# Performance work log

Hardware: AMD Instinct MI355X
Metric: run time of the kernel (lower is better)

The kernel has to match this reference:

```python
import jax, jax.numpy as jnp
import numpy as np

H = 256  # hidden_size


def _lstm_cell(x, h, c, Wih, Whh, b):
    # PyTorch gate order: input, forget, cell(g), output
    gates = x @ Wih.T + h @ Whh.T + b  # (B, 4H)
    i, f, g, o = jnp.split(gates, 4, axis=-1)
    c_new = jax.nn.sigmoid(f) * c + jax.nn.sigmoid(i) * jnp.tanh(g)
    h_new = jax.nn.sigmoid(o) * jnp.tanh(c_new)
    return h_new, c_new


def setup_inputs() -> dict:
    key = jax.random.key(0)
    ks = jax.random.split(key, 9)
    B, D_in, T, H4 = 64, 64, 1024, 4 * H
    s = 0.05  # keep gates out of saturation
    return {
        "x": jax.random.normal(ks[0], (B, D_in, T), jnp.float32),
        # layer 0: input size 64; layers 1-2: input size 2*H (bidirectional concat)
        "Wih0": jax.random.normal(ks[1], (2, H4, D_in), jnp.float32) * s,
        "Whh0": jax.random.normal(ks[2], (2, H4, H), jnp.float32) * s,
        "b0": jax.random.normal(ks[3], (2, H4), jnp.float32) * s,  # b_ih + b_hh fused
        "Wih12": jax.random.normal(ks[4], (2, 2, H4, 2 * H), jnp.float32) * s,
        "Whh12": jax.random.normal(ks[5], (2, 2, H4, H), jnp.float32) * s,
        "b12": jax.random.normal(ks[6], (2, 2, H4), jnp.float32) * s,
        # Conv1d(1, 81, (256,1)) == per-timestep linear over the hidden dim
        "conv_w": jax.random.normal(ks[7], (81, H), jnp.float32) * s,
        "conv_b": jax.random.normal(ks[8], (81,), jnp.float32) * s,
    }


def reference(x, Wih0, Whh0, b0, Wih12, Whh12, b12, conv_w, conv_b):
    B = x.shape[0]
    seq = jnp.transpose(x, (2, 0, 1))  # (T, B, D_in) like x.permute(2,0,1)
    h0 = jnp.zeros((6, B, H), x.dtype)  # num_layers * num_directions = 6
    c0 = jnp.zeros((6, B, H), x.dtype)

    def step(carry, x_t):
        h, c = carry
        hs, cs = [], []
        inp = x_t  # single timestep fed to the (bi)LSTM: both dirs see the same input
        for l in range(3):
            outs = []
            for d in range(2):
                idx = 2 * l + d
                if l == 0:
                    Wih, Whh, b = Wih0[d], Whh0[d], b0[d]
                else:
                    Wih, Whh, b = Wih12[l - 1, d], Whh12[l - 1, d], b12[l - 1, d]
                hn, cn = _lstm_cell(inp, h[idx], c[idx], Wih, Whh, b)
                outs.append(hn)
                hs.append(hn)
                cs.append(cn)
            inp = jnp.concatenate(outs, axis=-1)  # (B, 2H) into next layer
        new_h = jnp.stack(hs)
        new_c = jnp.stack(cs)
        # h.view(L, 2, B, H)[-1, -1]: last layer, backward direction
        return (new_h, new_c), hs[-1]

    _, ys = jax.lax.scan(step, (h0, c0), seq)  # ys: (T, B, H)

    # y.permute(1,2,0).unsqueeze(1) -> conv (256,1) kernel -> squeeze(2):
    # logits[b, o, t] = sum_h conv_w[o, h] * ys[t, b, h] + conv_b[o]
    logits = jnp.einsum('tbh,oh->bot', ys, conv_w) + conv_b[None, :, None]
    probs = jax.nn.softmax(logits, axis=1)
    return jnp.argmax(probs, axis=1)  # (B, T) int
```

## Files before the change

### kernel.cpp

```cpp
#include <hip/hip_runtime.h>


#define H_ 256
#define B_ 64
#define T_ 1024
#define NBLK 256
#define NTHR 1024
#define HBUF 98304
#define NTICK 1026

#define OFF_GEN  0
#define OFF_ROOT 64
#define OFF_CNT  128
#define OFF_H    4096
#define OFF_XT   1048576
#define OFF_YS   17825792

__device__ __forceinline__ float sigf(float x) {
  return 1.0f / (1.0f + __expf(-x));
}
__device__ __forceinline__ float tanhf_(float x) {
  float e = __expf(-2.0f * fabsf(x));
  float r = (1.0f - e) / (1.0f + e);
  return x >= 0.0f ? r : -r;
}

__device__ __forceinline__ void llc_ld1(const float4* p, float4& r) {
  asm volatile(
      "global_load_dwordx4 %0, %1, off sc0 sc1\n\t"
      "s_waitcnt vmcnt(0)"
      : "=v"(r)
      : "v"(p)
      : "memory");
}
__device__ __forceinline__ void llc_ld4(const float4* p, float4& r0, float4& r1,
                                        float4& r2, float4& r3) {
  asm volatile(
      "global_load_dwordx4 %0, %4, off sc0 sc1\n\t"
      "global_load_dwordx4 %1, %4, off offset:1024 sc0 sc1\n\t"
      "global_load_dwordx4 %2, %4, off offset:2048 sc0 sc1\n\t"
      "global_load_dwordx4 %3, %4, off offset:3072 sc0 sc1\n\t"
      "s_waitcnt vmcnt(0)"
      : "=&v"(r0), "=&v"(r1), "=&v"(r2), "=&v"(r3)
      : "v"(p)
      : "memory");
}
__device__ __forceinline__ void llc_ld8(const float4* p, const float4* q,
                                        float4& r0, float4& r1, float4& r2,
                                        float4& r3, float4& r4, float4& r5,
                                        float4& r6, float4& r7) {
  asm volatile(
      "global_load_dwordx4 %0, %8, off sc0 sc1\n\t"
      "global_load_dwordx4 %1, %8, off offset:1024 sc0 sc1\n\t"
      "global_load_dwordx4 %2, %8, off offset:2048 sc0 sc1\n\t"
      "global_load_dwordx4 %3, %8, off offset:3072 sc0 sc1\n\t"
      "global_load_dwordx4 %4, %9, off sc0 sc1\n\t"
      "global_load_dwordx4 %5, %9, off offset:1024 sc0 sc1\n\t"
      "global_load_dwordx4 %6, %9, off offset:2048 sc0 sc1\n\t"
      "global_load_dwordx4 %7, %9, off offset:3072 sc0 sc1\n\t"
      "s_waitcnt vmcnt(0)"
      : "=&v"(r0), "=&v"(r1), "=&v"(r2), "=&v"(r3), "=&v"(r4), "=&v"(r5),
        "=&v"(r6), "=&v"(r7)
      : "v"(p), "v"(q)
      : "memory");
}
__device__ __forceinline__ void llc_st_f2(float* p, float2 v) {
  asm volatile("global_store_dwordx2 %0, %1, off sc0 sc1" ::"v"(p), "v"(v)
               : "memory");
}

__global__ __launch_bounds__(64) void transpose_x(const float* __restrict__ x,
                                                  float* __restrict__ xT) {
  __shared__ float tile[64][65];
  const int k = blockIdx.y;
  const int t0 = blockIdx.x * 64;
  const int lane = threadIdx.x;
  for (int bi = 0; bi < 64; ++bi)
    tile[bi][lane] = x[bi * 65536 + k * 1024 + t0 + lane];
  __syncthreads();
  for (int ti = 0; ti < 64; ++ti)
    xT[(size_t)(t0 + ti) * 4096 + (k >> 2) * 256 + lane * 4 + (k & 3)] =
        tile[lane][ti];
}

__device__ __forceinline__ void body8(float* __restrict__ acc, const float4 av,
                                      const float* __restrict__ wl,
                                      const int k4) {
  const float* wp = wl + (size_t)k4 * 32;
#pragma unroll
  for (int a = 0; a < 8; ++a) {
    float4 wq = *(const float4*)(wp + a * 4);
    acc[a] = fmaf(wq.w, av.w,
                  fmaf(wq.z, av.z, fmaf(wq.y, av.y, fmaf(wq.x, av.x, acc[a]))));
  }
}

__device__ __forceinline__ void runLLC(float* __restrict__ acc,
                                       const float4* __restrict__ bufbase,
                                       const int bufk4, const int wk4,
                                       const int n,
                                       const float* __restrict__ wl,
                                       const int lane) {
  const float4* p = bufbase + (size_t)bufk4 * 64 + lane;
  int k = 0;
  for (; k + 8 <= n; k += 8) {
    float4 v0, v1, v2, v3, v4, v5, v6, v7;
    llc_ld8(p, p + 256, v0, v1, v2, v3, v4, v5, v6, v7);
    p += 512;
    body8(acc, v0, wl, wk4 + k + 0);
    body8(acc, v1, wl, wk4 + k + 1);
    body8(acc, v2, wl, wk4 + k + 2);
    body8(acc, v3, wl, wk4 + k + 3);
    body8(acc, v4, wl, wk4 + k + 4);
    body8(acc, v5, wl, wk4 + k + 5);
    body8(acc, v6, wl, wk4 + k + 6);
    body8(acc, v7, wl, wk4 + k + 7);
  }
  for (; k + 4 <= n; k += 4) {
    float4 v0, v1, v2, v3;
    llc_ld4(p, v0, v1, v2, v3);
    p += 256;
    body8(acc, v0, wl, wk4 + k + 0);
    body8(acc, v1, wl, wk4 + k + 1);
    body8(acc, v2, wl, wk4 + k + 2);
    body8(acc, v3, wl, wk4 + k + 3);
  }
  for (; k < n; ++k) {
    float4 v;
    llc_ld1(p, v);
    p += 64;
    body8(acc, v, wl, wk4 + k);
  }
}

__device__ __forceinline__ void runCached(float* __restrict__ acc,
                                          const float4* __restrict__ bufbase,
                                          const int bufk4, const int wk4,
                                          const int n,
                                          const float* __restrict__ wl,
                                          const int lane) {
  const float4* p = bufbase + (size_t)bufk4 * 64 + lane;
  int k = 0;
  for (; k + 4 <= n; k += 4) {
    float4 v0 = p[0], v1 = p[64], v2 = p[128], v3 = p[192];
    p += 256;
    body8(acc, v0, wl, wk4 + k + 0);
    body8(acc, v1, wl, wk4 + k + 1);
    body8(acc, v2, wl, wk4 + k + 2);
    body8(acc, v3, wl, wk4 + k + 3);
  }
  for (; k < n; ++k) {
    float4 v = *p;
    p += 64;
    body8(acc, v, wl, wk4 + k);
  }
}

__global__ __launch_bounds__(NTHR, 1) void lstm_persistent(
    const float* __restrict__ Wih0, const float* __restrict__ Whh0,
    const float* __restrict__ b0, const float* __restrict__ Wih12,
    const float* __restrict__ Whh12, const float* __restrict__ b12, char* wsb) {
  unsigned* gen = (unsigned*)(wsb + OFF_GEN);
  unsigned* root = (unsigned*)(wsb + OFF_ROOT);
  float* hb = (float*)(wsb + OFF_H);
  const float* xT = (const float*)(wsb + OFF_XT);
  float* ys = (float*)(wsb + OFF_YS);

  __shared__ float red[16][64][12];
  __shared__ float cst[3][2][64];
  __shared__ float wlds[14848];
  __shared__ float blds[3][8];

  const int bid = blockIdx.x;
  const int tid = threadIdx.x;
  const int lane = tid & 63;
  const int w = __builtin_amdgcn_readfirstlane(tid >> 6);
  const int d = bid >> 7;
  const int u0 = (bid & 127) * 2;

  if (tid < 384) ((float*)cst)[tid] = 0.f;

  auto stage = [&](const float* wA, int wAs, const float* wB, int wBs,
                   int K4s, int NA4s, float* dst) {
    const int nq = K4s * 8;
    for (int idx = tid; idx < nq; idx += NTHR) {
      const int a = idx / K4s;
      const int k4 = idx - a * K4s;
      const int row = (a & 3) * 256 + u0 + (a >> 2);
      const float* src = (k4 < NA4s) ? (wA + (size_t)row * wAs + k4 * 4)
                                     : (wB + (size_t)row * wBs + (k4 - NA4s) * 4);
      float4 q = *(const float4*)src;
      *(float4*)(dst + ((size_t)k4 * 8 + a) * 4) = q;
    }
  };
  stage(Wih0 + (size_t)d * 65536, 64, Whh0 + (size_t)d * 262144, 256, 80, 16,
        wlds);
  stage(Wih12 + (size_t)d * 524288, 512, Whh12 + (size_t)d * 262144, 256, 192,
        128, wlds + 2560);
  stage(Wih12 + (size_t)(2 + d) * 524288, 512,
        Whh12 + (size_t)(2 + d) * 262144, 256, 192, 128, wlds + 8704);
  if (tid < 24) {
    const int cell = tid >> 3, a = tid & 7;
    const float* bb = (cell == 0) ? (b0 + d * 1024)
                                  : ((cell == 1) ? (b12 + d * 1024)
                                                 : (b12 + (2 + d) * 1024));
    blds[cell][a] = bb[(a & 3) * 256 + u0 + (a >> 2)];
  }
  __syncthreads();

  unsigned* mycnt = (unsigned*)(wsb + OFF_CNT + (size_t)(bid & 7) * 64);

  for (unsigned tick = 0; tick < NTICK; ++tick) {
    const float* R = hb + ((tick + 1) & 1) * HBUF;
    float* W = hb + (tick & 1) * HBUF;
    const float4* Rf4 = (const float4*)R;

    const bool has0 = tick < 1024;
    const bool has1 = tick >= 1 && tick < 1025;
    const bool has2 = tick >= 2;

    float acc[8] = {0.f, 0.f, 0.f, 0.f, 0.f, 0.f, 0.f, 0.f};

    if (w < 4) {
      if (has0) {
        if (w == 0) {
          runCached(acc, (const float4*)xT + (size_t)tick * 1024, 0, 0, 16,
                    wlds, lane);
          runLLC(acc, Rf4 + (size_t)d * 4096, 0, 16, 4, wlds, lane);
        } else {
          const int lo = 20 * w;
          runLLC(acc, Rf4 + (size_t)d * 4096, lo - 16, lo, 20, wlds, lane);
        }
      }
    } else if (w < 10) {
      if (has1) {
        const int wi = w - 4, lo = 32 * wi;
        if (wi < 4)
          runLLC(acc, Rf4, lo, lo, 32, wlds + 2560, lane);
        else
          runLLC(acc, Rf4 + (size_t)(2 + d) * 4096, lo - 128, lo, 32,
                 wlds + 2560, lane);
      }
    } else {
      if (has2) {
        const int wi = w - 10, lo = 32 * wi;
        if (wi < 4)
          runLLC(acc, Rf4 + (size_t)2 * 4096, lo, lo, 32, wlds + 8704, lane);
        else
          runLLC(acc, Rf4 + (size_t)(4 + d) * 4096, lo - 128, lo, 32,
                 wlds + 8704, lane);
      }
    }

    *(float4*)&red[w][lane][0] = make_float4(acc[0], acc[1], acc[2], acc[3]);
    *(float4*)&red[w][lane][4] = make_float4(acc[4], acc[5], acc[6], acc[7]);
    __syncthreads();

    if (tid < 192) {
      const int cell = tid >> 6, b = tid & 63;
      const bool present = (cell == 0) ? has0 : ((cell == 1) ? has1 : has2);
      if (present) {
        const int w0 = (cell == 0) ? 0 : ((cell == 1) ? 4 : 10);
        const int nw = (cell == 0) ? 4 : 6;
        float g0 = blds[cell][0], g1 = blds[cell][1], g2 = blds[cell][2],
              g3 = blds[cell][3], g4 = blds[cell][4], g5 = blds[cell][5],
              g6 = blds[cell][6], g7 = blds[cell][7];
        for (int ww = w0; ww < w0 + nw; ++ww) {
          const float4* rp = (const float4*)&red[ww][b][0];
          float4 s0 = rp[0], s1 = rp[1];
          g0 += s0.x; g1 += s0.y; g2 += s0.z; g3 += s0.w;
          g4 += s1.x; g5 += s1.y; g6 += s1.z; g7 += s1.w;
        }
        const float iv0 = sigf(g0), fv0 = sigf(g1), gv0 = tanhf_(g2),
                    ov0 = sigf(g3);
        const float iv1 = sigf(g4), fv1 = sigf(g5), gv1 = tanhf_(g6),
                    ov1 = sigf(g7);
        float c0 = fv0 * cst[cell][0][b] + iv0 * gv0;
        float c1 = fv1 * cst[cell][1][b] + iv1 * gv1;
        cst[cell][0][b] = c0;
        cst[cell][1][b] = c1;
        const float h0 = ov0 * tanhf_(c0), h1 = ov1 * tanhf_(c1);
        const int cellidx = (cell == 0) ? d : ((cell == 1) ? (2 + d) : (4 + d));
        float* hp =
            W + (size_t)cellidx * 16384 + (u0 >> 2) * 256 + b * 4 + (u0 & 3);
        llc_st_f2(hp, make_float2(h0, h1));
        if (cell == 2 && d == 1) {
          *(float2*)(ys + (size_t)((int)tick - 2) * 16384 + b * 256 + u0) =
              make_float2(h0, h1);
        }
      }
    }
    asm volatile("s_waitcnt vmcnt(0)" ::: "memory");
    __syncthreads();

    if (tid == 0) {
      unsigned old = __hip_atomic_fetch_add(mycnt, 1u, __ATOMIC_RELAXED,
                                            __HIP_MEMORY_SCOPE_AGENT);
      if (old == (tick + 1) * (NBLK / 8) - 1) {
        unsigned r = __hip_atomic_fetch_add(root, 1u, __ATOMIC_RELAXED,
                                            __HIP_MEMORY_SCOPE_AGENT);
        if (r == (tick + 1) * 8 - 1) {
          __hip_atomic_store(gen, tick + 1, __ATOMIC_RELAXED,
                             __HIP_MEMORY_SCOPE_AGENT);
        }
      }
      while (__hip_atomic_load(gen, __ATOMIC_RELAXED, __HIP_MEMORY_SCOPE_AGENT) <
             tick + 1) {
        __builtin_amdgcn_s_sleep(2);
      }
    }
    __syncthreads();
  }
}

__global__ __launch_bounds__(256) void conv_argmax(const float* __restrict__ yst,
                                                   const float* __restrict__ cw,
                                                   const float* __restrict__ cb,
                                                   int* __restrict__ out) {
  const int t = blockIdx.x;
  const int tid = threadIdx.x, lane = tid & 63, w = tid >> 6;
  const float* yrow = yst + (size_t)t * (B_ * H_) + lane * H_;
  float best = -3.4e38f;
  int bi = 0;
  for (int og = 0; og < 3; ++og) {
    float acc[8];
    int ov[8];
#pragma unroll
    for (int m = 0; m < 8; ++m) {
      int o = w + 32 * og + 4 * m;
      ov[m] = (o < 81) ? o : 80;
      acc[m] = (o < 81) ? cb[o] : -3.4e38f;
    }
    for (int uu = 0; uu < H_; uu += 4) {
      float4 y4 = *(const float4*)(yrow + uu);
#pragma unroll
      for (int m = 0; m < 8; ++m) {
        const float* wr = cw + ov[m] * H_ + uu;
        acc[m] += wr[0] * y4.x + wr[1] * y4.y + wr[2] * y4.z + wr[3] * y4.w;
      }
    }
#pragma unroll
    for (int m = 0; m < 8; ++m) {
      int o = w + 32 * og + 4 * m;
      if (o < 81 && acc[m] > best) {
        best = acc[m];
        bi = o;
      }
    }
  }
  __shared__ float sv[4][64];
  __shared__ int si[4][64];
  sv[w][lane] = best;
  si[w][lane] = bi;
  __syncthreads();
  if (tid < 64) {
    float bv = sv[0][tid];
    int bo = si[0][tid];
#pragma unroll
    for (int ww = 1; ww < 4; ++ww) {
      float v = sv[ww][tid];
      int o = si[ww][tid];
      if (v > bv || (v == bv && o < bo)) {
        bv = v;
        bo = o;
      }
    }
    out[tid * T_ + t] = bo;
  }
}

extern "C" void kernel_launch(void* const* d_in, const int* in_sizes, int n_in,
                              void* d_out, int out_size, void* d_ws,
                              size_t ws_size, hipStream_t stream) {
  const float* x = (const float*)d_in[0];
  const float* Wih0 = (const float*)d_in[1];
  const float* Whh0 = (const float*)d_in[2];
  const float* b0 = (const float*)d_in[3];
  const float* Wih12 = (const float*)d_in[4];
  const float* Whh12 = (const float*)d_in[5];
  const float* b12 = (const float*)d_in[6];
  const float* cw = (const float*)d_in[7];
  const float* cb = (const float*)d_in[8];
  int* out = (int*)d_out;
  char* wsb = (char*)d_ws;

  hipMemsetAsync(wsb, 0, OFF_H + 786432, stream);
  transpose_x<<<dim3(16, 64, 1), dim3(64, 1, 1), 0, stream>>>(
      x, (float*)(wsb + OFF_XT));
  lstm_persistent<<<dim3(NBLK, 1, 1), dim3(NTHR, 1, 1), 0, stream>>>(
      Wih0, Whh0, b0, Wih12, Whh12, b12, wsb);
  conv_argmax<<<dim3(T_, 1, 1), dim3(256, 1, 1), 0, stream>>>(
      (const float*)(wsb + OFF_YS), cw, cb, out);
}
```

Before: 15.62 ms.

## Retile LSTM blocks to 4 units x 32 batch and stream layer-0 weights from global

Each persistent block now owns 4 hidden units for half the batch instead of 2 units for the full batch. The two lanes halves of each wave work on different unit pairs. Layers 1-2 weights are staged into the larger LDS footprint with a 16-row interleave. Layer-0 weights are no longer kept in LDS and are read directly from global memory, so they rely on caching. The goal is to halve the recurrent h-vector traffic each block reads per tick. The cost is that layer-0 weight loads go through global/L2 with strided rows instead of LDS.

```diff
diff --git a/kernel.cpp b/kernel.cpp
--- a/kernel.cpp
+++ b/kernel.cpp
@@ -86,10 +86,22 @@
 __device__ __forceinline__ void body8(float* __restrict__ acc, const float4 av,
                                       const float* __restrict__ wl,
                                       const int k4) {
-  const float* wp = wl + (size_t)k4 * 32;
+  const float* wp = wl + (size_t)k4 * 64;
 #pragma unroll
   for (int a = 0; a < 8; ++a) {
     float4 wq = *(const float4*)(wp + a * 4);
+    acc[a] = fmaf(wq.w, av.w,
+                  fmaf(wq.z, av.z, fmaf(wq.y, av.y, fmaf(wq.x, av.x, acc[a]))));
+  }
+}
+
+__device__ __forceinline__ void body8g(float* __restrict__ acc, const float4 av,
+                                       const float* __restrict__ gw,
+                                       const int stride, const int kk) {
+#pragma unroll
+  for (int a = 0; a < 8; ++a) {
+    const float* wp = gw + (size_t)(((a & 3) * 256 + (a >> 2)) * stride) + kk * 4;
+    float4 wq = *(const float4*)wp;
     acc[a] = fmaf(wq.w, av.w,
                   fmaf(wq.z, av.z, fmaf(wq.y, av.y, fmaf(wq.x, av.x, acc[a]))));
   }
@@ -100,8 +112,8 @@
                                        const int bufk4, const int wk4,
                                        const int n,
                                        const float* __restrict__ wl,
-                                       const int lane) {
-  const float4* p = bufbase + (size_t)bufk4 * 64 + lane;
+                                       const int laneA) {
+  const float4* p = bufbase + (size_t)bufk4 * 64 + laneA;
   int k = 0;
   for (; k + 8 <= n; k += 8) {
     float4 v0, v1, v2, v3, v4, v5, v6, v7;
@@ -133,32 +145,68 @@
   }
 }
 
-__device__ __forceinline__ void runCached(float* __restrict__ acc,
-                                          const float4* __restrict__ bufbase,
-                                          const int bufk4, const int wk4,
-                                          const int n,
-                                          const float* __restrict__ wl,
-                                          const int lane) {
-  const float4* p = bufbase + (size_t)bufk4 * 64 + lane;
+__device__ __forceinline__ void runLLC0(float* __restrict__ acc,
+                                        const float4* __restrict__ bufbase,
+                                        const int bufk4, const int n,
+                                        const float* __restrict__ gw,
+                                        const int laneA) {
+  const float4* p = bufbase + (size_t)bufk4 * 64 + laneA;
+  int k = 0;
+  for (; k + 8 <= n; k += 8) {
+    float4 v0, v1, v2, v3, v4, v5, v6, v7;
+    llc_ld8(p, p + 256, v0, v1, v2, v3, v4, v5, v6, v7);
+    p += 512;
+    body8g(acc, v0, gw, 256, bufk4 + k + 0);
+    body8g(acc, v1, gw, 256, bufk4 + k + 1);
+    body8g(acc, v2, gw, 256, bufk4 + k + 2);
+    body8g(acc, v3, gw, 256, bufk4 + k + 3);
+    body8g(acc, v4, gw, 256, bufk4 + k + 4);
+    body8g(acc, v5, gw, 256, bufk4 + k + 5);
+    body8g(acc, v6, gw, 256, bufk4 + k + 6);
+    body8g(acc, v7, gw, 256, bufk4 + k + 7);
+  }
+  for (; k + 4 <= n; k += 4) {
+    float4 v0, v1, v2, v3;
+    llc_ld4(p, v0, v1, v2, v3);
+    p += 256;
+    body8g(acc, v0, gw, 256, bufk4 + k + 0);
+    body8g(acc, v1, gw, 256, bufk4 + k + 1);
+    body8g(acc, v2, gw, 256, bufk4 + k + 2);
+    body8g(acc, v3, gw, 256, bufk4 + k + 3);
+  }
+  for (; k < n; ++k) {
+    float4 v;
+    llc_ld1(p, v);
+    p += 64;
+    body8g(acc, v, gw, 256, bufk4 + k);
+  }
+}
+
+__device__ __forceinline__ void runCached0(float* __restrict__ acc,
+                                           const float4* __restrict__ bufbase,
+                                           const int n,
+                                           const float* __restrict__ gw,
+                                           const int laneA) {
+  const float4* p = bufbase + laneA;
   int k = 0;
   for (; k + 4 <= n; k += 4) {
     float4 v0 = p[0], v1 = p[64], v2 = p[128], v3 = p[192];
     p += 256;
-    body8(acc, v0, wl, wk4 + k + 0);
-    body8(acc, v1, wl, wk4 + k + 1);
-    body8(acc, v2, wl, wk4 + k + 2);
-    body8(acc, v3, wl, wk4 + k + 3);
+    body8g(acc, v0, gw, 64, k + 0);
+    body8g(acc, v1, gw, 64, k + 1);
+    body8g(acc, v2, gw, 64, k + 2);
+    body8g(acc, v3, gw, 64, k + 3);
   }
   for (; k < n; ++k) {
     float4 v = *p;
     p += 64;
-    body8(acc, v, wl, wk4 + k);
+    body8g(acc, v, gw, 64, k);
   }
 }
 
 __global__ __launch_bounds__(NTHR, 1) void lstm_persistent(
     const float* __restrict__ Wih0, const float* __restrict__ Whh0,
-    const float* __restrict__ b0, const float* __restrict__ Wih12,
+    const float* __restrict__ b0v, const float* __restrict__ Wih12,
     const float* __restrict__ Whh12, const float* __restrict__ b12, char* wsb) {
   unsigned* gen = (unsigned*)(wsb + OFF_GEN);
   unsigned* root = (unsigned*)(wsb + OFF_ROOT);
@@ -167,44 +215,55 @@
   float* ys = (float*)(wsb + OFF_YS);
 
   __shared__ float red[16][64][12];
-  __shared__ float cst[3][2][64];
-  __shared__ float wlds[14848];
-  __shared__ float blds[3][8];
+  __shared__ float cst[3][2][2][32];
+  __shared__ float wlds[24576];
+  __shared__ float blds[3][2][8];
 
   const int bid = blockIdx.x;
   const int tid = threadIdx.x;
   const int lane = tid & 63;
   const int w = __builtin_amdgcn_readfirstlane(tid >> 6);
   const int d = bid >> 7;
-  const int u0 = (bid & 127) * 2;
-
-  if (tid < 384) ((float*)cst)[tid] = 0.f;
-
-  auto stage = [&](const float* wA, int wAs, const float* wB, int wBs,
-                   int K4s, int NA4s, float* dst) {
-    const int nq = K4s * 8;
+  const int tile = (bid & 127) >> 1;
+  const int half = bid & 1;
+  const int u0 = tile * 4;
+  const int bOff = half * 32;
+
+  const int up = lane >> 5;
+  const int laneA = bOff + (lane & 31);
+  const int uB = u0 + up * 2;
+
+  const float* gx = Wih0 + (size_t)d * 65536 + (size_t)uB * 64;
+  const float* gr = Whh0 + (size_t)d * 262144 + (size_t)uB * 256;
+  const float* wlh1 = wlds + (up << 5);
+  const float* wlh2 = wlds + 12288 + (up << 5);
+
+  if (tid < 384) (((float*)cst))[tid] = 0.f;
+
+  auto stage16 = [&](const float* wA, int wAs, const float* wB, int wBs,
+                     int K4s, int NA4s, float* dst) {
+    const int nq = K4s * 16;
     for (int idx = tid; idx < nq; idx += NTHR) {
-      const int a = idx / K4s;
-      const int k4 = idx - a * K4s;
-      const int row = (a & 3) * 256 + u0 + (a >> 2);
+      const int a16 = idx / K4s;
+      const int k4 = idx - a16 * K4s;
+      const int upS = a16 >> 3, a = a16 & 7;
+      const int row = (a & 3) * 256 + u0 + upS * 2 + (a >> 2);
       const float* src = (k4 < NA4s) ? (wA + (size_t)row * wAs + k4 * 4)
                                      : (wB + (size_t)row * wBs + (k4 - NA4s) * 4);
       float4 q = *(const float4*)src;
-      *(float4*)(dst + ((size_t)k4 * 8 + a) * 4) = q;
+      *(float4*)(dst + ((size_t)k4 * 16 + a16) * 4) = q;
     }
   };
-  stage(Wih0 + (size_t)d * 65536, 64, Whh0 + (size_t)d * 262144, 256, 80, 16,
-        wlds);
-  stage(Wih12 + (size_t)d * 524288, 512, Whh12 + (size_t)d * 262144, 256, 192,
-        128, wlds + 2560);
-  stage(Wih12 + (size_t)(2 + d) * 524288, 512,
-        Whh12 + (size_t)(2 + d) * 262144, 256, 192, 128, wlds + 8704);
-  if (tid < 24) {
-    const int cell = tid >> 3, a = tid & 7;
-    const float* bb = (cell == 0) ? (b0 + d * 1024)
+  stage16(Wih12 + (size_t)d * 524288, 512, Whh12 + (size_t)d * 262144, 256,
+          192, 128, wlds);
+  stage16(Wih12 + (size_t)(2 + d) * 524288, 512,
+          Whh12 + (size_t)(2 + d) * 262144, 256, 192, 128, wlds + 12288);
+  if (tid < 48) {
+    const int cell = tid >> 4, rest = tid & 15, upB = rest >> 3, a = rest & 7;
+    const float* bb = (cell == 0) ? (b0v + d * 1024)
                                   : ((cell == 1) ? (b12 + d * 1024)
                                                  : (b12 + (2 + d) * 1024));
-    blds[cell][a] = bb[(a & 3) * 256 + u0 + (a >> 2)];
+    blds[cell][upB][a] = bb[(a & 3) * 256 + u0 + upB * 2 + (a >> 2)];
   }
   __syncthreads();
 
@@ -224,31 +283,30 @@
     if (w < 4) {
       if (has0) {
         if (w == 0) {
-          runCached(acc, (const float4*)xT + (size_t)tick * 1024, 0, 0, 16,
-                    wlds, lane);
-          runLLC(acc, Rf4 + (size_t)d * 4096, 0, 16, 4, wlds, lane);
+          runCached0(acc, (const float4*)xT + (size_t)tick * 1024, 16, gx,
+                     laneA);
+          runLLC0(acc, Rf4 + (size_t)d * 4096, 0, 4, gr, laneA);
         } else {
-          const int lo = 20 * w;
-          runLLC(acc, Rf4 + (size_t)d * 4096, lo - 16, lo, 20, wlds, lane);
+          runLLC0(acc, Rf4 + (size_t)d * 4096, 20 * w - 16, 20, gr, laneA);
         }
       }
     } else if (w < 10) {
       if (has1) {
         const int wi = w - 4, lo = 32 * wi;
         if (wi < 4)
-          runLLC(acc, Rf4, lo, lo, 32, wlds + 2560, lane);
+          runLLC(acc, Rf4, lo, lo, 32, wlh1, laneA);
         else
-          runLLC(acc, Rf4 + (size_t)(2 + d) * 4096, lo - 128, lo, 32,
-                 wlds + 2560, lane);
+          runLLC(acc, Rf4 + (size_t)(2 + d) * 4096, lo - 128, lo, 32, wlh1,
+                 laneA);
       }
     } else {
       if (has2) {
         const int wi = w - 10, lo = 32 * wi;
         if (wi < 4)
-          runLLC(acc, Rf4 + (size_t)2 * 4096, lo, lo, 32, wlds + 8704, lane);
+          runLLC(acc, Rf4 + (size_t)2 * 4096, lo, lo, 32, wlh2, laneA);
         else
-          runLLC(acc, Rf4 + (size_t)(4 + d) * 4096, lo - 128, lo, 32,
-                 wlds + 8704, lane);
+          runLLC(acc, Rf4 + (size_t)(4 + d) * 4096, lo - 128, lo, 32, wlh2,
+                 laneA);
       }
     }
 
@@ -257,16 +315,18 @@
     __syncthreads();
 
     if (tid < 192) {
-      const int cell = tid >> 6, b = tid & 63;
+      const int cell = tid >> 6, sub = tid & 63;
+      const int upE = sub >> 5, b = sub & 31;
       const bool present = (cell == 0) ? has0 : ((cell == 1) ? has1 : has2);
       if (present) {
         const int w0 = (cell == 0) ? 0 : ((cell == 1) ? 4 : 10);
         const int nw = (cell == 0) ? 4 : 6;
-        float g0 = blds[cell][0], g1 = blds[cell][1], g2 = blds[cell][2],
-              g3 = blds[cell][3], g4 = blds[cell][4], g5 = blds[cell][5],
-              g6 = blds[cell][6], g7 = blds[cell][7];
+        float g0 = blds[cell][upE][0], g1 = blds[cell][upE][1],
+              g2 = blds[cell][upE][2], g3 = blds[cell][upE][3],
+              g4 = blds[cell][upE][4], g5 = blds[cell][upE][5],
+              g6 = blds[cell][upE][6], g7 = blds[cell][upE][7];
         for (int ww = w0; ww < w0 + nw; ++ww) {
-          const float4* rp = (const float4*)&red[ww][b][0];
+          const float4* rp = (const float4*)&red[ww][sub][0];
           float4 s0 = rp[0], s1 = rp[1];
           g0 += s0.x; g1 += s0.y; g2 += s0.z; g3 += s0.w;
           g4 += s1.x; g5 += s1.y; g6 += s1.z; g7 += s1.w;
@@ -275,18 +335,18 @@
                     ov0 = sigf(g3);
         const float iv1 = sigf(g4), fv1 = sigf(g5), gv1 = tanhf_(g6),
                     ov1 = sigf(g7);
-        float c0 = fv0 * cst[cell][0][b] + iv0 * gv0;
-        float c1 = fv1 * cst[cell][1][b] + iv1 * gv1;
-        cst[cell][0][b] = c0;
-        cst[cell][1][b] = c1;
+        float c0 = fv0 * cst[cell][upE][0][b] + iv0 * gv0;
+        float c1 = fv1 * cst[cell][upE][1][b] + iv1 * gv1;
+        cst[cell][upE][0][b] = c0;
+        cst[cell][upE][1][b] = c1;
         const float h0 = ov0 * tanhf_(c0), h1 = ov1 * tanhf_(c1);
         const int cellidx = (cell == 0) ? d : ((cell == 1) ? (2 + d) : (4 + d));
-        float* hp =
-            W + (size_t)cellidx * 16384 + (u0 >> 2) * 256 + b * 4 + (u0 & 3);
+        float* hp = W + (size_t)cellidx * 16384 + (u0 >> 2) * 256 +
+                    (bOff + b) * 4 + upE * 2;
         llc_st_f2(hp, make_float2(h0, h1));
         if (cell == 2 && d == 1) {
-          *(float2*)(ys + (size_t)((int)tick - 2) * 16384 + b * 256 + u0) =
-              make_float2(h0, h1);
+          *(float2*)(ys + (size_t)((int)tick - 2) * 16384 + (bOff + b) * 256 +
+                     u0 + upE * 2) = make_float2(h0, h1);
         }
       }
     }
```

Result: slower. 16.47 ms (+5.4%).
